# Performance work log

Hardware: AMD Instinct MI355X
Metric: run time of the kernel (lower is better)

Reference implementation:

```python
import jax, jax.numpy as jnp
import numpy as np

NUM_HEADS = 16
LN_EPS = 1e-5


def setup_inputs() -> dict:
    key = jax.random.key(0)
    ks = jax.random.split(key, 5)
    B, S, E = 4, 1024, 1024
    x = jax.random.normal(ks[0], (B, S, E), dtype=jnp.float32)
    # Linear weights stored torch-style [out, in]; scaled for stable softmax
    Wq = jax.random.normal(ks[1], (E, E), dtype=jnp.float32) * (E ** -0.5)
    Wk = jax.random.normal(ks[2], (E, E), dtype=jnp.float32) * (E ** -0.5)
    Wv = jax.random.normal(ks[3], (E, E), dtype=jnp.float32) * (E ** -0.5)
    Wo = jax.random.normal(ks[4], (E, E), dtype=jnp.float32) * (E ** -0.5)
    gamma = jnp.ones((E,), dtype=jnp.float32)
    beta = jnp.zeros((E,), dtype=jnp.float32)
    return {"x": x, "Wq": Wq, "Wk": Wk, "Wv": Wv, "Wo": Wo, "gamma": gamma, "beta": beta}


def reference(x, Wq, Wk, Wv, Wo, gamma, beta):
    B, S, E = x.shape
    H = NUM_HEADS
    D = E // H
    scale = 1.0 / (D ** 0.5)

    q = x @ Wq.T                      # [B,S,E]
    k = (x @ Wk.T) * scale            # [B,S,E]
    v = x @ Wv.T                      # [B,S,E]

    qh = q.reshape(B, S, H, D)
    kh = k.reshape(B, S, H, D)
    qk = jnp.einsum('bthd,bshd->bhts', qh, kh)        # [B,H,T,S]

    causal = jnp.tril(jnp.ones((S, S), dtype=bool))   # mask==0 -> -inf
    qk = jnp.where(causal, qk, -jnp.inf)
    attn = jax.nn.softmax(qk, axis=-1)                # [B,H,T,S]

    # Faithful to torch.unflatten(v, dim=2, sizes=[-1, num_heads]):
    # heads are the LAST axis of the value split (transposed vs q/k).
    vh = v.reshape(B, S, D, H)                        # [B,S,D,H]
    # einsum 'kjlm,kmij->kiml': out[b,t,h,d] = sum_s vh[b,s,d,h]*attn[b,h,t,s]
    qkv = jnp.einsum('bsdh,bhts->bthd', vh, attn)     # [B,T,H,D]
    qkv = qkv.reshape(B, S, E)

    # LayerNorm over last dim
    mu = jnp.mean(qkv, axis=-1, keepdims=True)
    var = jnp.mean(jnp.square(qkv - mu), axis=-1, keepdims=True)
    ln = (qkv - mu) * jax.lax.rsqrt(var + LN_EPS) * gamma + beta

    return ln @ Wo.T
```

## Files before the change

### kernel.cpp

```cpp
#include <hip/hip_runtime.h>
#include <stdint.h>


using bf16x8 = __attribute__((ext_vector_type(8))) short;
using f32x4  = __attribute__((ext_vector_type(4))) float;
using u16x8  = __attribute__((ext_vector_type(8))) unsigned short;

#define AS1 __attribute__((address_space(1)))
#define AS3 __attribute__((address_space(3)))

__device__ __forceinline__ void gload16(const void* g, void* l) {
  __builtin_amdgcn_global_load_lds((const AS1 uint32_t*)g, (AS3 uint32_t*)l, 16, 0, 0);
}

__device__ __forceinline__ unsigned short f2bf(float f) {
  union { float f; uint32_t u; } v; v.f = f;
  uint32_t u = v.u + 0x7fffu + ((v.u >> 16) & 1u);
  return (unsigned short)(u >> 16);
}
__device__ __forceinline__ float bf2f(unsigned short h) {
  union { uint32_t u; float f; } v; v.u = ((uint32_t)h) << 16;
  return v.f;
}

__global__ void cvt_bf16(const float* __restrict__ in, unsigned short* __restrict__ out,
                         int n4, float scale) {
  int i = blockIdx.x * blockDim.x + threadIdx.x;
  if (i >= n4) return;
  float4 v = reinterpret_cast<const float4*>(in)[i];
  ushort4 o;
  o.x = f2bf(v.x * scale);
  o.y = f2bf(v.y * scale);
  o.z = f2bf(v.z * scale);
  o.w = f2bf(v.w * scale);
  reinterpret_cast<ushort4*>(out)[i] = o;
}

template<int OUTF32>
__global__ __launch_bounds__(256, 2) void gemm_bt(const unsigned short* __restrict__ A,
                                                  const unsigned short* __restrict__ B,
                                                  void* __restrict__ Cv,
                                                  int M, int N, int K) {
  (void)M;
  __shared__ __align__(16) unsigned short lA[128 * 32];
  __shared__ __align__(16) unsigned short lB[128 * 32];
  const int tn_cnt = N >> 7;
  const int nwg = gridDim.x;
  int bid = (int)blockIdx.x;
  int bid2 = (bid & 7) * (nwg >> 3) + (bid >> 3);
  int tm = bid2 / tn_cnt, tn = bid2 % tn_cnt;
  int t = (int)threadIdx.x;
  int w = t >> 6, lane = t & 63, lr = lane & 15, hi = lane >> 4;
  int wr = w >> 1, wc = w & 1;
  int srow = t >> 2, scol = (t & 3) << 3;
  const unsigned short* a0 = A + (size_t)(tm * 128 + srow) * K + scol;
  const unsigned short* a1 = a0 + (size_t)64 * K;
  const unsigned short* b0 = B + (size_t)(tn * 128 + srow) * K + scol;
  const unsigned short* b1 = b0 + (size_t)64 * K;
  char* dA0 = (char*)lA + w * 1024;
  char* dA1 = (char*)lA + 4096 + w * 1024;
  char* dB0 = (char*)lB + w * 1024;
  char* dB1 = (char*)lB + 4096 + w * 1024;
  f32x4 acc[4][4] = {};
  for (int k0 = 0; k0 < K; k0 += 32) {
    __syncthreads();
    gload16(a0 + k0, dA0);
    gload16(a1 + k0, dA1);
    gload16(b0 + k0, dB0);
    gload16(b1 + k0, dB1);
    __syncthreads();
    bf16x8 af[4], bfr[4];
#pragma unroll
    for (int mi = 0; mi < 4; ++mi)
      af[mi] = *reinterpret_cast<const bf16x8*>(&lA[(wr * 64 + mi * 16 + lr) * 32 + hi * 8]);
#pragma unroll
    for (int ni = 0; ni < 4; ++ni)
      bfr[ni] = *reinterpret_cast<const bf16x8*>(&lB[(wc * 64 + ni * 16 + lr) * 32 + hi * 8]);
#pragma unroll
    for (int mi = 0; mi < 4; ++mi)
#pragma unroll
      for (int ni = 0; ni < 4; ++ni)
        acc[mi][ni] = __builtin_amdgcn_mfma_f32_16x16x32_bf16(af[mi], bfr[ni], acc[mi][ni], 0, 0, 0);
  }
#pragma unroll
  for (int mi = 0; mi < 4; ++mi) {
#pragma unroll
    for (int r = 0; r < 4; ++r) {
      size_t row = (size_t)(tm * 128 + wr * 64 + mi * 16 + hi * 4 + r);
#pragma unroll
      for (int ni = 0; ni < 4; ++ni) {
        int col = tn * 128 + wc * 64 + ni * 16 + lr;
        float v = acc[mi][ni][r];
        if (OUTF32) reinterpret_cast<float*>(Cv)[row * N + col] = v;
        else        reinterpret_cast<unsigned short*>(Cv)[row * N + col] = f2bf(v);
      }
    }
  }
}

__global__ __launch_bounds__(256) void vrepack(const unsigned short* __restrict__ QKV,
                                               unsigned short* __restrict__ VhT) {
  __shared__ __align__(16) unsigned short lT[64 * 72];
  int st = (int)blockIdx.x;
  int ct = (int)blockIdx.y;
  int b  = (int)blockIdx.z;
  int t = (int)threadIdx.x;
#pragma unroll
  for (int i = 0; i < 2; ++i) {
    int c = i * 256 + t;
    int row = c >> 3, ch = c & 7;
    u16x8 v = *reinterpret_cast<const u16x8*>(
        QKV + (size_t)(b * 1024 + st * 64 + row) * 3072 + 2048 + ct * 64 + ch * 8);
    *reinterpret_cast<u16x8*>(&lT[row * 72 + ch * 8]) = v;
  }
  __syncthreads();
#pragma unroll
  for (int i = 0; i < 2; ++i) {
    int c2 = i * 256 + t;
    int cl = c2 >> 3, ch = c2 & 7;
    int h = cl & 15;
    int d = ct * 4 + (cl >> 4);
    u16x8 v;
#pragma unroll
    for (int j = 0; j < 8; ++j) v[j] = lT[(ch * 8 + j) * 72 + cl];
    *reinterpret_cast<u16x8*>(
        VhT + (size_t)((b * 16 + h) * 64 + d) * 1024 + st * 64 + ch * 8) = v;
  }
}

__global__ __launch_bounds__(256, 2) void attn_fwd(const unsigned short* __restrict__ QKV,
                                                   const unsigned short* __restrict__ VhT,
                                                   unsigned short* __restrict__ Out) {
  __shared__ __align__(16) unsigned short lQ[128 * 64];
  __shared__ __align__(16) unsigned short lK[64 * 64];
  __shared__ __align__(16) unsigned short lV[64 * 64];
  __shared__ __align__(16) unsigned short lP[4][32 * 64];
  int bid = (int)blockIdx.x;
  int qt = 7 - (bid & 7);
  int bh = bid >> 3;
  int b = bh >> 4, h = bh & 15;
  int t = (int)threadIdx.x;
  int w = t >> 6, lane = t & 63, lr = lane & 15, hi = lane >> 4;
  (void)lane;
#pragma unroll
  for (int i = 0; i < 4; ++i) {
    int c = i * 256 + t;
    int row = c >> 3, slot = c & 7;
    gload16(QKV + (size_t)(b * 1024 + qt * 128 + row) * 3072 + h * 64 + ((slot ^ (row & 7)) << 3),
            (char*)lQ + i * 4096 + w * 1024);
  }
  __syncthreads();
  bf16x8 qfr[2][2];
#pragma unroll
  for (int qf = 0; qf < 2; ++qf)
#pragma unroll
    for (int kc = 0; kc < 2; ++kc) {
      int row = w * 32 + qf * 16 + lr;
      int slot = (kc * 4 + hi) ^ (row & 7);
      qfr[qf][kc] = *reinterpret_cast<const bf16x8*>((const char*)lQ + row * 128 + slot * 16);
    }
  int qbase = qt * 128 + w * 32;
  f32x4 o[2][4] = {};
  float mrun[2][4], lpart[2][4];
#pragma unroll
  for (int qf = 0; qf < 2; ++qf)
#pragma unroll
    for (int r = 0; r < 4; ++r) { mrun[qf][r] = -1e30f; lpart[qf][r] = 0.f; }
  int nkb = 2 * qt + 2;
  for (int kb = 0; kb < nkb; ++kb) {
    __syncthreads();
#pragma unroll
    for (int i = 0; i < 2; ++i) {
      int c = i * 256 + t;
      int row = c >> 3, slot = c & 7;
      gload16(QKV + (size_t)(b * 1024 + kb * 64 + row) * 3072 + 1024 + h * 64 + ((slot ^ (row & 7)) << 3),
              (char*)lK + i * 4096 + w * 1024);
    }
#pragma unroll
    for (int i = 0; i < 2; ++i) {
      int c = i * 256 + t;
      int row = c >> 3, slot = c & 7;
      gload16(VhT + (size_t)(bh * 64 + row) * 1024 + kb * 64 + ((slot ^ (row & 7)) << 3),
              (char*)lV + i * 4096 + w * 1024);
    }
    __syncthreads();
    if (kb * 64 > qbase + 31) continue;
    bf16x8 kfr[4][2];
#pragma unroll
    for (int nf = 0; nf < 4; ++nf)
#pragma unroll
      for (int kc = 0; kc < 2; ++kc) {
        int row = nf * 16 + lr;
        int slot = (kc * 4 + hi) ^ (row & 7);
        kfr[nf][kc] = *reinterpret_cast<const bf16x8*>((const char*)lK + row * 128 + slot * 16);
      }
    f32x4 s[2][4] = {};
#pragma unroll
    for (int qf = 0; qf < 2; ++qf)
#pragma unroll
      for (int nf = 0; nf < 4; ++nf)
#pragma unroll
        for (int kc = 0; kc < 2; ++kc)
          s[qf][nf] = __builtin_amdgcn_mfma_f32_16x16x32_bf16(qfr[qf][kc], kfr[nf][kc], s[qf][nf], 0, 0, 0);
    if (kb * 64 + 63 > qbase) {
#pragma unroll
      for (int qf = 0; qf < 2; ++qf)
#pragma unroll
        for (int nf = 0; nf < 4; ++nf)
#pragma unroll
          for (int r = 0; r < 4; ++r) {
            int q = qbase + qf * 16 + hi * 4 + r;
            int kv = kb * 64 + nf * 16 + lr;
            if (kv > q) s[qf][nf][r] = -1e30f;
          }
    }
#pragma unroll
    for (int qf = 0; qf < 2; ++qf) {
      float rm[4];
#pragma unroll
      for (int r = 0; r < 4; ++r)
        rm[r] = fmaxf(fmaxf(s[qf][0][r], s[qf][1][r]), fmaxf(s[qf][2][r], s[qf][3][r]));
#pragma unroll
      for (int r = 0; r < 4; ++r) {
        rm[r] = fmaxf(rm[r], __shfl_xor(rm[r], 1));
        rm[r] = fmaxf(rm[r], __shfl_xor(rm[r], 2));
        rm[r] = fmaxf(rm[r], __shfl_xor(rm[r], 4));
        rm[r] = fmaxf(rm[r], __shfl_xor(rm[r], 8));
      }
#pragma unroll
      for (int r = 0; r < 4; ++r) {
        float mn = fmaxf(mrun[qf][r], rm[r]);
        float al = __expf(mrun[qf][r] - mn);
        mrun[qf][r] = mn;
        float ps = 0.f;
#pragma unroll
        for (int nf = 0; nf < 4; ++nf) {
          float p = __expf(s[qf][nf][r] - mn);
          s[qf][nf][r] = p;
          ps += p;
        }
        lpart[qf][r] = lpart[qf][r] * al + ps;
#pragma unroll
        for (int df = 0; df < 4; ++df) o[qf][df][r] *= al;
      }
    }
    char* pb = (char*)lP[w];
#pragma unroll
    for (int qf = 0; qf < 2; ++qf)
#pragma unroll
      for (int nf = 0; nf < 4; ++nf)
#pragma unroll
        for (int r = 0; r < 4; ++r) {
          int rp = qf * 16 + hi * 4 + r;
          int col = nf * 16 + lr;
          int slot = (col >> 3) ^ (rp & 7);
          *reinterpret_cast<unsigned short*>(pb + rp * 128 + slot * 16 + (col & 7) * 2) =
              f2bf(s[qf][nf][r]);
        }
    asm volatile("s_waitcnt lgkmcnt(0)" ::: "memory");
    __builtin_amdgcn_sched_barrier(0);
    bf16x8 pfr[2][2], vfr[4][2];
#pragma unroll
    for (int qf = 0; qf < 2; ++qf)
#pragma unroll
      for (int kc = 0; kc < 2; ++kc) {
        int row = qf * 16 + lr;
        int slot = (kc * 4 + hi) ^ (row & 7);
        pfr[qf][kc] = *reinterpret_cast<const bf16x8*>(pb + row * 128 + slot * 16);
      }
#pragma unroll
    for (int df = 0; df < 4; ++df)
#pragma unroll
      for (int kc = 0; kc < 2; ++kc) {
        int row = df * 16 + lr;
        int slot = (kc * 4 + hi) ^ (row & 7);
        vfr[df][kc] = *reinterpret_cast<const bf16x8*>((const char*)lV + row * 128 + slot * 16);
      }
#pragma unroll
    for (int qf = 0; qf < 2; ++qf)
#pragma unroll
      for (int df = 0; df < 4; ++df)
#pragma unroll
        for (int kc = 0; kc < 2; ++kc)
          o[qf][df] = __builtin_amdgcn_mfma_f32_16x16x32_bf16(pfr[qf][kc], vfr[df][kc], o[qf][df], 0, 0, 0);
  }
#pragma unroll
  for (int qf = 0; qf < 2; ++qf)
#pragma unroll
    for (int r = 0; r < 4; ++r) {
      float l = lpart[qf][r];
      l += __shfl_xor(l, 1);
      l += __shfl_xor(l, 2);
      l += __shfl_xor(l, 4);
      l += __shfl_xor(l, 8);
      float inv = 1.0f / l;
      int qrow = qbase + qf * 16 + hi * 4 + r;
#pragma unroll
      for (int df = 0; df < 4; ++df)
        Out[(size_t)(b * 1024 + qrow) * 1024 + h * 64 + df * 16 + lr] = f2bf(o[qf][df][r] * inv);
    }
}

__global__ __launch_bounds__(256) void lnorm(const unsigned short* __restrict__ X,
                                             unsigned short* __restrict__ Y,
                                             const float* __restrict__ gamma,
                                             const float* __restrict__ beta) {
  int rowi = (int)blockIdx.x * 4 + ((int)threadIdx.x >> 6);
  int lane = (int)threadIdx.x & 63;
  const unsigned short* row = X + (size_t)rowi * 1024;
  u16x8 v0 = reinterpret_cast<const u16x8*>(row)[lane];
  u16x8 v1 = reinterpret_cast<const u16x8*>(row)[lane + 64];
  float f0[8], f1[8];
  float s = 0.f, sq = 0.f;
#pragma unroll
  for (int j = 0; j < 8; ++j) {
    f0[j] = bf2f(v0[j]); f1[j] = bf2f(v1[j]);
    s  += f0[j] + f1[j];
    sq += f0[j] * f0[j] + f1[j] * f1[j];
  }
#pragma unroll
  for (int m = 1; m <= 32; m <<= 1) { s += __shfl_xor(s, m); sq += __shfl_xor(sq, m); }
  float mean = s * (1.0f / 1024.0f);
  float var  = sq * (1.0f / 1024.0f) - mean * mean;
  float rstd = rsqrtf(var + 1e-5f);
  int c0 = lane * 8, c1 = 512 + lane * 8;
  u16x8 o0, o1;
#pragma unroll
  for (int j = 0; j < 8; ++j) {
    o0[j] = f2bf((f0[j] - mean) * rstd * gamma[c0 + j] + beta[c0 + j]);
    o1[j] = f2bf((f1[j] - mean) * rstd * gamma[c1 + j] + beta[c1 + j]);
  }
  reinterpret_cast<u16x8*>(Y + (size_t)rowi * 1024)[lane]      = o0;
  reinterpret_cast<u16x8*>(Y + (size_t)rowi * 1024)[lane + 64] = o1;
}

extern "C" void kernel_launch(void* const* d_in, const int* in_sizes, int n_in,
                              void* d_out, int out_size, void* d_ws, size_t ws_size,
                              hipStream_t stream) {
  (void)in_sizes; (void)n_in; (void)out_size; (void)ws_size;
  const float* x     = (const float*)d_in[0];
  const float* Wq    = (const float*)d_in[1];
  const float* Wk    = (const float*)d_in[2];
  const float* Wv    = (const float*)d_in[3];
  const float* Wo    = (const float*)d_in[4];
  const float* gamma = (const float*)d_in[5];
  const float* beta  = (const float*)d_in[6];
  char* ws = (char*)d_ws;
  unsigned short* xb   = (unsigned short*)(ws);
  unsigned short* wcat = (unsigned short*)(ws + (8u  << 20));
  unsigned short* wob  = (unsigned short*)(ws + (14u << 20));
  unsigned short* qkv  = (unsigned short*)(ws + (16u << 20));
  unsigned short* vht  = (unsigned short*)(ws + (40u << 20));
  unsigned short* att  = (unsigned short*)(ws + (48u << 20));
  unsigned short* lnb  = (unsigned short*)(ws + (56u << 20));

  cvt_bf16<<<4096, 256, 0, stream>>>(x,  xb,              1048576, 1.0f);
  cvt_bf16<<<1024, 256, 0, stream>>>(Wq, wcat,             262144, 1.0f);
  cvt_bf16<<<1024, 256, 0, stream>>>(Wk, wcat + 1048576,   262144, 0.125f);
  cvt_bf16<<<1024, 256, 0, stream>>>(Wv, wcat + 2097152,   262144, 1.0f);
  cvt_bf16<<<1024, 256, 0, stream>>>(Wo, wob,              262144, 1.0f);
  gemm_bt<0><<<768, 256, 0, stream>>>(xb, wcat, qkv, 4096, 3072, 1024);
  vrepack<<<dim3(16, 16, 4), 256, 0, stream>>>(qkv, vht);
  attn_fwd<<<512, 256, 0, stream>>>(qkv, vht, att);
  lnorm<<<1024, 256, 0, stream>>>(att, lnb, gamma, beta);
  gemm_bt<1><<<256, 256, 0, stream>>>(lnb, wob, (void*)d_out, 4096, 1024, 1024);
}
```

Before: 205.7 us.

## Double-buffer K/V tiles in attention and fuse input conversion kernels

```diff
diff --git a/kernel.cpp b/kernel.cpp
--- a/kernel.cpp
+++ b/kernel.cpp
@@ -23,17 +23,28 @@
   return v.f;
 }
 
-__global__ void cvt_bf16(const float* __restrict__ in, unsigned short* __restrict__ out,
-                         int n4, float scale) {
-  int i = blockIdx.x * blockDim.x + threadIdx.x;
-  if (i >= n4) return;
-  float4 v = reinterpret_cast<const float4*>(in)[i];
+__global__ __launch_bounds__(256) void cvt_all(const float* __restrict__ x,
+                                               const float* __restrict__ Wq,
+                                               const float* __restrict__ Wk,
+                                               const float* __restrict__ Wv,
+                                               const float* __restrict__ Wo,
+                                               unsigned short* __restrict__ xb,
+                                               unsigned short* __restrict__ wcat,
+                                               unsigned short* __restrict__ wob) {
+  int i = (int)blockIdx.x * 256 + (int)threadIdx.x;
+  const float* src; unsigned short* dst; int off; float scale = 1.0f;
+  if (i < 1048576)      { src = x;  dst = xb;             off = i; }
+  else if (i < 1310720) { src = Wq; dst = wcat;           off = i - 1048576; }
+  else if (i < 1572864) { src = Wk; dst = wcat + 1048576; off = i - 1310720; scale = 0.125f; }
+  else if (i < 1835008) { src = Wv; dst = wcat + 2097152; off = i - 1572864; }
+  else                  { src = Wo; dst = wob;            off = i - 1835008; }
+  float4 v = reinterpret_cast<const float4*>(src)[off];
   ushort4 o;
   o.x = f2bf(v.x * scale);
   o.y = f2bf(v.y * scale);
   o.z = f2bf(v.z * scale);
   o.w = f2bf(v.w * scale);
-  reinterpret_cast<ushort4*>(out)[i] = o;
+  reinterpret_cast<ushort4*>(dst)[off] = o;
 }
 
 template<int OUTF32>
@@ -132,16 +143,35 @@
                                                    const unsigned short* __restrict__ VhT,
                                                    unsigned short* __restrict__ Out) {
   __shared__ __align__(16) unsigned short lQ[128 * 64];
-  __shared__ __align__(16) unsigned short lK[64 * 64];
-  __shared__ __align__(16) unsigned short lV[64 * 64];
+  __shared__ __align__(16) unsigned short lK[2][64 * 64];
+  __shared__ __align__(16) unsigned short lV[2][64 * 64];
   __shared__ __align__(16) unsigned short lP[4][32 * 64];
   int bid = (int)blockIdx.x;
-  int qt = 7 - (bid & 7);
-  int bh = bid >> 3;
+  int half = bid >> 8, idx = bid & 255;
+  int bh = idx >> 2, jj = idx & 3;
+  int qt = half ? jj : 7 - jj;
   int b = bh >> 4, h = bh & 15;
   int t = (int)threadIdx.x;
   int w = t >> 6, lane = t & 63, lr = lane & 15, hi = lane >> 4;
   (void)lane;
+
+  auto stageKV = [&](int kb, int buf) {
+#pragma unroll
+    for (int i = 0; i < 2; ++i) {
+      int c = i * 256 + t;
+      int row = c >> 3, slot = c & 7;
+      gload16(QKV + (size_t)(b * 1024 + kb * 64 + row) * 3072 + 1024 + h * 64 + ((slot ^ (row & 7)) << 3),
+              (char*)lK + buf * 8192 + i * 4096 + w * 1024);
+    }
+#pragma unroll
+    for (int i = 0; i < 2; ++i) {
+      int c = i * 256 + t;
+      int row = c >> 3, slot = c & 7;
+      gload16(VhT + (size_t)(bh * 64 + row) * 1024 + kb * 64 + ((slot ^ (row & 7)) << 3),
+              (char*)lV + buf * 8192 + i * 4096 + w * 1024);
+    }
+  };
+
 #pragma unroll
   for (int i = 0; i < 4; ++i) {
     int c = i * 256 + t;
@@ -149,7 +179,9 @@
     gload16(QKV + (size_t)(b * 1024 + qt * 128 + row) * 3072 + h * 64 + ((slot ^ (row & 7)) << 3),
             (char*)lQ + i * 4096 + w * 1024);
   }
+  stageKV(0, 0);
   __syncthreads();
+
   bf16x8 qfr[2][2];
 #pragma unroll
   for (int qf = 0; qf < 2; ++qf)
@@ -166,124 +198,117 @@
   for (int qf = 0; qf < 2; ++qf)
 #pragma unroll
     for (int r = 0; r < 4; ++r) { mrun[qf][r] = -1e30f; lpart[qf][r] = 0.f; }
+
   int nkb = 2 * qt + 2;
   for (int kb = 0; kb < nkb; ++kb) {
+    int cur = kb & 1;
+    if (kb + 1 < nkb) stageKV(kb + 1, cur ^ 1);
+    if (kb * 64 <= qbase + 31) {
+      const char* kbuf = (const char*)lK + cur * 8192;
+      const char* vbuf = (const char*)lV + cur * 8192;
+      bf16x8 kfr[4][2];
+#pragma unroll
+      for (int nf = 0; nf < 4; ++nf)
+#pragma unroll
+        for (int kc = 0; kc < 2; ++kc) {
+          int row = nf * 16 + lr;
+          int slot = (kc * 4 + hi) ^ (row & 7);
+          kfr[nf][kc] = *reinterpret_cast<const bf16x8*>(kbuf + row * 128 + slot * 16);
+        }
+      f32x4 s[2][4] = {};
+#pragma unroll
+      for (int qf = 0; qf < 2; ++qf)
+#pragma unroll
+        for (int nf = 0; nf < 4; ++nf)
+#pragma unroll
+          for (int kc = 0; kc < 2; ++kc)
+            s[qf][nf] = __builtin_amdgcn_mfma_f32_16x16x32_bf16(qfr[qf][kc], kfr[nf][kc], s[qf][nf], 0, 0, 0);
+      bf16x8 vfr[4][2];
+#pragma unroll
+      for (int df = 0; df < 4; ++df)
+#pragma unroll
+        for (int kc = 0; kc < 2; ++kc) {
+          int row = df * 16 + lr;
+          int slot = (kc * 4 + hi) ^ (row & 7);
+          vfr[df][kc] = *reinterpret_cast<const bf16x8*>(vbuf + row * 128 + slot * 16);
+        }
+      if (kb * 64 + 63 > qbase) {
+#pragma unroll
+        for (int qf = 0; qf < 2; ++qf)
+#pragma unroll
+          for (int nf = 0; nf < 4; ++nf)
+#pragma unroll
+            for (int r = 0; r < 4; ++r) {
+              int q = qbase + qf * 16 + hi * 4 + r;
+              int kv = kb * 64 + nf * 16 + lr;
+              if (kv > q) s[qf][nf][r] = -1e30f;
+            }
+      }
+#pragma unroll
+      for (int qf = 0; qf < 2; ++qf) {
+        float rm[4];
+#pragma unroll
+        for (int r = 0; r < 4; ++r)
+          rm[r] = fmaxf(fmaxf(s[qf][0][r], s[qf][1][r]), fmaxf(s[qf][2][r], s[qf][3][r]));
+#pragma unroll
+        for (int r = 0; r < 4; ++r) {
+          rm[r] = fmaxf(rm[r], __shfl_xor(rm[r], 1));
+          rm[r] = fmaxf(rm[r], __shfl_xor(rm[r], 2));
+          rm[r] = fmaxf(rm[r], __shfl_xor(rm[r], 4));
+          rm[r] = fmaxf(rm[r], __shfl_xor(rm[r], 8));
+        }
+#pragma unroll
+        for (int r = 0; r < 4; ++r) {
+          float mn = fmaxf(mrun[qf][r], rm[r]);
+          float al = __expf(mrun[qf][r] - mn);
+          mrun[qf][r] = mn;
+          float ps = 0.f;
+#pragma unroll
+          for (int nf = 0; nf < 4; ++nf) {
+            float p = __expf(s[qf][nf][r] - mn);
+            s[qf][nf][r] = p;
+            ps += p;
+          }
+          lpart[qf][r] = lpart[qf][r] * al + ps;
+#pragma unroll
+          for (int df = 0; df < 4; ++df) o[qf][df][r] *= al;
+        }
+      }
+      char* pb = (char*)lP[w];
+#pragma unroll
+      for (int qf = 0; qf < 2; ++qf)
+#pragma unroll
+        for (int nf = 0; nf < 4; ++nf)
+#pragma unroll
+          for (int r = 0; r < 4; ++r) {
+            int rp = qf * 16 + hi * 4 + r;
+            int col = nf * 16 + lr;
+            int slot = (col >> 3) ^ (rp & 7);
+            *reinterpret_cast<unsigned short*>(pb + rp * 128 + slot * 16 + (col & 7) * 2) =
+                f2bf(s[qf][nf][r]);
+          }
+      asm volatile("s_waitcnt lgkmcnt(0)" ::: "memory");
+      __builtin_amdgcn_sched_barrier(0);
+      bf16x8 pfr[2][2];
+#pragma unroll
+      for (int qf = 0; qf < 2; ++qf)
+#pragma unroll
+        for (int kc = 0; kc < 2; ++kc) {
+          int row = qf * 16 + lr;
+          int slot = (kc * 4 + hi) ^ (row & 7);
+          pfr[qf][kc] = *reinterpret_cast<const bf16x8*>(pb + row * 128 + slot * 16);
+        }
+#pragma unroll
+      for (int qf = 0; qf < 2; ++qf)
+#pragma unroll
+        for (int df = 0; df < 4; ++df)
+#pragma unroll
+          for (int kc = 0; kc < 2; ++kc)
+            o[qf][df] = __builtin_amdgcn_mfma_f32_16x16x32_bf16(pfr[qf][kc], vfr[df][kc], o[qf][df], 0, 0, 0);
+    }
     __syncthreads();
-#pragma unroll
-    for (int i = 0; i < 2; ++i) {
-      int c = i * 256 + t;
-      int row = c >> 3, slot = c & 7;
-      gload16(QKV + (size_t)(b * 1024 + kb * 64 + row) * 3072 + 1024 + h * 64 + ((slot ^ (row & 7)) << 3),
-              (char*)lK + i * 4096 + w * 1024);
-    }
-#pragma unroll
-    for (int i = 0; i < 2; ++i) {
-      int c = i * 256 + t;
-      int row = c >> 3, slot = c & 7;
-      gload16(VhT + (size_t)(bh * 64 + row) * 1024 + kb * 64 + ((slot ^ (row & 7)) << 3),
-              (char*)lV + i * 4096 + w * 1024);
-    }
-    __syncthreads();
-    if (kb * 64 > qbase + 31) continue;
-    bf16x8 kfr[4][2];
-#pragma unroll
-    for (int nf = 0; nf < 4; ++nf)
-#pragma unroll
-      for (int kc = 0; kc < 2; ++kc) {
-        int row = nf * 16 + lr;
-        int slot = (kc * 4 + hi) ^ (row & 7);
-        kfr[nf][kc] = *reinterpret_cast<const bf16x8*>((const char*)lK + row * 128 + slot * 16);
-      }
-    f32x4 s[2][4] = {};
-#pragma unroll
-    for (int qf = 0; qf < 2; ++qf)
-#pragma unroll
-      for (int nf = 0; nf < 4; ++nf)
-#pragma unroll
-        for (int kc = 0; kc < 2; ++kc)
-          s[qf][nf] = __builtin_amdgcn_mfma_f32_16x16x32_bf16(qfr[qf][kc], kfr[nf][kc], s[qf][nf], 0, 0, 0);
-    if (kb * 64 + 63 > qbase) {
-#pragma unroll
-      for (int qf = 0; qf < 2; ++qf)
-#pragma unroll
-        for (int nf = 0; nf < 4; ++nf)
-#pragma unroll
-          for (int r = 0; r < 4; ++r) {
-            int q = qbase + qf * 16 + hi * 4 + r;
-            int kv = kb * 64 + nf * 16 + lr;
-            if (kv > q) s[qf][nf][r] = -1e30f;
-          }
-    }
-#pragma unroll
-    for (int qf = 0; qf < 2; ++qf) {
-      float rm[4];
-#pragma unroll
-      for (int r = 0; r < 4; ++r)
-        rm[r] = fmaxf(fmaxf(s[qf][0][r], s[qf][1][r]), fmaxf(s[qf][2][r], s[qf][3][r]));
-#pragma unroll
-      for (int r = 0; r < 4; ++r) {
-        rm[r] = fmaxf(rm[r], __shfl_xor(rm[r], 1));
-        rm[r] = fmaxf(rm[r], __shfl_xor(rm[r], 2));
-        rm[r] = fmaxf(rm[r], __shfl_xor(rm[r], 4));
-        rm[r] = fmaxf(rm[r], __shfl_xor(rm[r], 8));
-      }
-#pragma unroll
-      for (int r = 0; r < 4; ++r) {
-        float mn = fmaxf(mrun[qf][r], rm[r]);
-        float al = __expf(mrun[qf][r] - mn);
-        mrun[qf][r] = mn;
-        float ps = 0.f;
-#pragma unroll
-        for (int nf = 0; nf < 4; ++nf) {
-          float p = __expf(s[qf][nf][r] - mn);
-          s[qf][nf][r] = p;
-          ps += p;
-        }
-        lpart[qf][r] = lpart[qf][r] * al + ps;
-#pragma unroll
-        for (int df = 0; df < 4; ++df) o[qf][df][r] *= al;
-      }
-    }
-    char* pb = (char*)lP[w];
-#pragma unroll
-    for (int qf = 0; qf < 2; ++qf)
-#pragma unroll
-      for (int nf = 0; nf < 4; ++nf)
-#pragma unroll
-        for (int r = 0; r < 4; ++r) {
-          int rp = qf * 16 + hi * 4 + r;
-          int col = nf * 16 + lr;
-          int slot = (col >> 3) ^ (rp & 7);
-          *reinterpret_cast<unsigned short*>(pb + rp * 128 + slot * 16 + (col & 7) * 2) =
-              f2bf(s[qf][nf][r]);
-        }
-    asm volatile("s_waitcnt lgkmcnt(0)" ::: "memory");
-    __builtin_amdgcn_sched_barrier(0);
-    bf16x8 pfr[2][2], vfr[4][2];
-#pragma unroll
-    for (int qf = 0; qf < 2; ++qf)
-#pragma unroll
-      for (int kc = 0; kc < 2; ++kc) {
-        int row = qf * 16 + lr;
-        int slot = (kc * 4 + hi) ^ (row & 7);
-        pfr[qf][kc] = *reinterpret_cast<const bf16x8*>(pb + row * 128 + slot * 16);
-      }
-#pragma unroll
-    for (int df = 0; df < 4; ++df)
-#pragma unroll
-      for (int kc = 0; kc < 2; ++kc) {
-        int row = df * 16 + lr;
-        int slot = (kc * 4 + hi) ^ (row & 7);
-        vfr[df][kc] = *reinterpret_cast<const bf16x8*>((const char*)lV + row * 128 + slot * 16);
-      }
-#pragma unroll
-    for (int qf = 0; qf < 2; ++qf)
-#pragma unroll
-      for (int df = 0; df < 4; ++df)
-#pragma unroll
-        for (int kc = 0; kc < 2; ++kc)
-          o[qf][df] = __builtin_amdgcn_mfma_f32_16x16x32_bf16(pfr[qf][kc], vfr[df][kc], o[qf][df], 0, 0, 0);
-  }
+  }
+
 #pragma unroll
   for (int qf = 0; qf < 2; ++qf)
 #pragma unroll
@@ -354,11 +379,7 @@
   unsigned short* att  = (unsigned short*)(ws + (48u << 20));
   unsigned short* lnb  = (unsigned short*)(ws + (56u << 20));
 
-  cvt_bf16<<<4096, 256, 0, stream>>>(x,  xb,              1048576, 1.0f);
-  cvt_bf16<<<1024, 256, 0, stream>>>(Wq, wcat,             262144, 1.0f);
-  cvt_bf16<<<1024, 256, 0, stream>>>(Wk, wcat + 1048576,   262144, 0.125f);
-  cvt_bf16<<<1024, 256, 0, stream>>>(Wv, wcat + 2097152,   262144, 1.0f);
-  cvt_bf16<<<1024, 256, 0, stream>>>(Wo, wob,              262144, 1.0f);
+  cvt_all<<<8192, 256, 0, stream>>>(x, Wq, Wk, Wv, Wo, xb, wcat, wob);
   gemm_bt<0><<<768, 256, 0, stream>>>(xb, wcat, qkv, 4096, 3072, 1024);
   vrepack<<<dim3(16, 16, 4), 256, 0, stream>>>(qkv, vht);
   attn_fwd<<<512, 256, 0, stream>>>(qkv, vht, att);
```

Measured after the change: 190.2 us. -7.5%, faster.
